# Kernel tuning notes

Measured on AMD Instinct MI355X. Metric: run time of the kernel, lower is better.

Reference implementation:

```python
import jax, jax.numpy as jnp
import numpy as np

B, S, D, H = 4, 2048, 1024, 16
DK = D // H
NEG = -1000000000.0


def setup_inputs() -> dict:
    key = jax.random.key(0)
    ks = jax.random.split(key, 12)
    scale = 1.0 / np.sqrt(D)
    inp = {
        "query": jax.random.normal(ks[0], (B, S, D), jnp.float32),
        "key": jax.random.normal(ks[1], (B, S, D), jnp.float32),
        "value": jax.random.normal(ks[2], (B, S, D), jnp.float32),
        "mask": jax.random.randint(ks[3], (B, S, S), 0, 2, jnp.int32),
        "Wq": jax.random.normal(ks[4], (D, D), jnp.float32) * scale,
        "bq": jnp.zeros((D,), jnp.float32),
        "Wk": jax.random.normal(ks[5], (D, D), jnp.float32) * scale,
        "bk": jnp.zeros((D,), jnp.float32),
        "Wv": jax.random.normal(ks[6], (D, D), jnp.float32) * scale,
        "bv": jnp.zeros((D,), jnp.float32),
        "Wo": jax.random.normal(ks[7], (D, D), jnp.float32) * scale,
        "bo": jnp.zeros((D,), jnp.float32),
    }
    return inp


def _split_heads(x):
    # (B, S, D) -> (B, H, S, DK)
    return x.reshape(B, -1, H, DK).transpose(0, 2, 1, 3)


def reference(query, key, value, mask, Wq, bq, Wk, bk, Wv, bv, Wo, bo):
    q = _split_heads(query @ Wq.T + bq)
    k = _split_heads(key @ Wk.T + bk)
    v = _split_heads(value @ Wv.T + bv)
    scores = jnp.einsum('bhqd,bhkd->bhqk', q, k) / jnp.sqrt(jnp.float32(DK))
    scores = jnp.where(mask[:, None, :, :] == 0, NEG, scores)
    p_attn = jax.nn.softmax(scores, axis=-1)
    x = jnp.einsum('bhqk,bhkd->bhqd', p_attn, v)
    x = x.transpose(0, 2, 1, 3).reshape(B, -1, D)
    return x @ Wo.T + bo
```

## Files before the change

### kernel.cpp

```cpp
#include <hip/hip_runtime.h>

#define BDIM 4
#define SDIM 2048
#define DDIM 1024
#define HDIM 16
#define DKDIM 64
#define MDIM (BDIM*SDIM)

typedef __attribute__((ext_vector_type(8))) short bf16x8_t;
typedef __attribute__((ext_vector_type(4))) float f32x4_t;
typedef __attribute__((ext_vector_type(16))) float f32x16_t;

__device__ __forceinline__ unsigned short f2bf(float f) {
    union { float f; unsigned u; } v; v.f = f;
    unsigned r = v.u + 0x7FFFu + ((v.u >> 16) & 1u);
    return (unsigned short)(r >> 16);
}

__device__ __forceinline__ unsigned pkbf(float a, float b) {
    unsigned r;
    asm("v_cvt_pk_bf16_f32 %0, %1, %2" : "=v"(r) : "v"(a), "v"(b));
    return r;
}

__device__ __forceinline__ void plswap(unsigned &a, unsigned &b) {
    asm("v_permlane32_swap_b32 %0, %1" : "+v"(a), "+v"(b));
}

#if defined(__has_builtin) && __has_builtin(__builtin_amdgcn_exp2f)
#define EXP2F(x) __builtin_amdgcn_exp2f(x)
#else
#define EXP2F(x) __expf((x) * 0.69314718f)
#endif

#if defined(__has_builtin) && __has_builtin(__builtin_amdgcn_sbfe)
#define SBFE1(x, p) __builtin_amdgcn_sbfe((int)(x), (p), 1)
#else
#define SBFE1(x, p) (((int)((x) << (31 - (p)))) >> 31)
#endif

#define QSCALE 0.18033688011112042f

__device__ __forceinline__ void gl_lds16(const void* g, void* l) {
    __builtin_amdgcn_global_load_lds(
        (const __attribute__((address_space(1))) unsigned int*)g,
        (__attribute__((address_space(3))) unsigned int*)l, 16, 0, 0);
}

__global__ void cvt3(const float* __restrict__ a, const float* __restrict__ b, const float* __restrict__ c,
                     unsigned short* __restrict__ oa, unsigned short* __restrict__ ob, unsigned short* __restrict__ oc,
                     int n4) {
    int i = blockIdx.x * blockDim.x + threadIdx.x;
    const float* s = blockIdx.y == 0 ? a : (blockIdx.y == 1 ? b : c);
    unsigned short* d = blockIdx.y == 0 ? oa : (blockIdx.y == 1 ? ob : oc);
    if (i < n4) {
        float4 v = ((const float4*)s)[i];
        uint2 o;
        o.x = pkbf(v.x, v.y);
        o.y = pkbf(v.z, v.w);
        ((uint2*)d)[i] = o;
    }
}

__global__ void cvt4(const float* __restrict__ a, const float* __restrict__ b,
                     const float* __restrict__ c, const float* __restrict__ e,
                     unsigned short* __restrict__ oa, unsigned short* __restrict__ ob,
                     unsigned short* __restrict__ oc, unsigned short* __restrict__ oe,
                     int n4) {
    int i = blockIdx.x * blockDim.x + threadIdx.x;
    const float* s = blockIdx.y == 0 ? a : (blockIdx.y == 1 ? b : (blockIdx.y == 2 ? c : e));
    unsigned short* d = blockIdx.y == 0 ? oa : (blockIdx.y == 1 ? ob : (blockIdx.y == 2 ? oc : oe));
    if (i < n4) {
        float4 v = ((const float4*)s)[i];
        uint2 o;
        o.x = pkbf(v.x, v.y);
        o.y = pkbf(v.z, v.w);
        ((uint2*)d)[i] = o;
    }
}

__global__ void pack_mask(const int* __restrict__ m, unsigned long long* __restrict__ bits) {
    int g = blockIdx.x * 256 + threadIdx.x;
    unsigned long long bal = __ballot(m[g] != 0);
    if ((threadIdx.x & 63) == 0) bits[g >> 6] = bal;
}

__global__ __launch_bounds__(256) void gemm_qkv(
    const unsigned short* __restrict__ A0, const unsigned short* __restrict__ A1,
    const unsigned short* __restrict__ A2,
    const unsigned short* __restrict__ B0, const unsigned short* __restrict__ B1,
    const unsigned short* __restrict__ B2,
    const float* __restrict__ bi0, const float* __restrict__ bi1, const float* __restrict__ bi2,
    unsigned short* __restrict__ C0, unsigned short* __restrict__ C1,
    unsigned short* __restrict__ C2)
{
    __shared__ unsigned short As[2][128 * 32];
    __shared__ unsigned short Bs[2][128 * 32];
    const int K = DDIM, M = MDIM, N = DDIM;
    const int bid = blockIdx.x;
    const int swz = (bid & 7) * 192 + (bid >> 3);
    const int z = swz >> 9;
    const int rem = swz & 511;
    const int bm = rem >> 3, bn = rem & 7;

    const unsigned short* A = z == 0 ? A0 : (z == 1 ? A1 : A2);
    const unsigned short* Bw = z == 0 ? B0 : (z == 1 ? B1 : B2);
    const float* bias = z == 0 ? bi0 : (z == 1 ? bi1 : bi2);
    unsigned short* Cb = z == 0 ? C0 : (z == 1 ? C1 : C2);
    const float scale = z == 0 ? QSCALE : 1.0f;

    const int tid = threadIdx.x;
    const int w = tid >> 6, lane = tid & 63;
    const int wr = w >> 1, wc = w & 1;
    const int quad = lane >> 4, l16 = lane & 15;

    const int rl = lane >> 2;
    const int cl = (((lane & 3) ^ ((rl >> 1) & 3)) * 8);
    const int sw = (l16 >> 1) & 3;
    const int c0 = w * 2;
    const unsigned short* gA = A + (size_t)(bm * 128 + c0 * 16 + rl) * K + cl;
    const unsigned short* gB = Bw + (size_t)(bn * 128 + c0 * 16 + rl) * K + cl;
    const int ldsoff = c0 * 512 + lane * 8;

    f32x4_t acc[4][4] = {};

    gl_lds16(gA, &As[0][ldsoff]);
    gl_lds16(gA + (size_t)16 * K, &As[0][ldsoff + 16 * 32]);
    gl_lds16(gB, &Bs[0][ldsoff]);
    gl_lds16(gB + (size_t)16 * K, &Bs[0][ldsoff + 16 * 32]);

    int cur = 0;
    for (int k0 = 0; k0 < K; k0 += 32) {
        __syncthreads();
        if (k0 + 32 < K) {
            const unsigned short* nA = gA + k0 + 32;
            const unsigned short* nB = gB + k0 + 32;
            gl_lds16(nA, &As[cur ^ 1][ldsoff]);
            gl_lds16(nA + (size_t)16 * K, &As[cur ^ 1][ldsoff + 16 * 32]);
            gl_lds16(nB, &Bs[cur ^ 1][ldsoff]);
            gl_lds16(nB + (size_t)16 * K, &Bs[cur ^ 1][ldsoff + 16 * 32]);
        }
        bf16x8_t af[4], bfr[4];
#pragma unroll
        for (int mi = 0; mi < 4; ++mi)
            af[mi] = *(const bf16x8_t*)(&As[cur][(wr * 64 + mi * 16 + l16) * 32 + (quad ^ sw) * 8]);
#pragma unroll
        for (int ni = 0; ni < 4; ++ni)
            bfr[ni] = *(const bf16x8_t*)(&Bs[cur][(wc * 64 + ni * 16 + l16) * 32 + (quad ^ sw) * 8]);
#pragma unroll
        for (int mi = 0; mi < 4; ++mi)
#pragma unroll
            for (int ni = 0; ni < 4; ++ni)
                acc[mi][ni] = __builtin_amdgcn_mfma_f32_16x16x32_bf16(bfr[ni], af[mi], acc[mi][ni], 0, 0, 0);
        cur ^= 1;
    }

    if (z == 2) {
#pragma unroll
        for (int mi = 0; mi < 4; ++mi) {
#pragma unroll
            for (int ni = 0; ni < 4; ++ni) {
                const int n0 = bn * 128 + wc * 64 + ni * 16 + quad * 4;
                const int m = bm * 128 + wr * 64 + mi * 16 + l16;
                const float4 bv4 = *(const float4*)&bias[n0];
                Cb[(size_t)(n0 + 0) * M + m] = f2bf(acc[mi][ni][0] + bv4.x);
                Cb[(size_t)(n0 + 1) * M + m] = f2bf(acc[mi][ni][1] + bv4.y);
                Cb[(size_t)(n0 + 2) * M + m] = f2bf(acc[mi][ni][2] + bv4.z);
                Cb[(size_t)(n0 + 3) * M + m] = f2bf(acc[mi][ni][3] + bv4.w);
            }
        }
    } else {
#pragma unroll
        for (int mi = 0; mi < 4; ++mi) {
#pragma unroll
            for (int ni = 0; ni < 4; ++ni) {
                const int n0 = bn * 128 + wc * 64 + ni * 16 + quad * 4;
                const int m = bm * 128 + wr * 64 + mi * 16 + l16;
                const float4 bv4 = *(const float4*)&bias[n0];
                uint2 pk2;
                pk2.x = pkbf((acc[mi][ni][0] + bv4.x) * scale, (acc[mi][ni][1] + bv4.y) * scale);
                pk2.y = pkbf((acc[mi][ni][2] + bv4.z) * scale, (acc[mi][ni][3] + bv4.w) * scale);
                *(uint2*)(Cb + (size_t)m * N + n0) = pk2;
            }
        }
    }
}

__global__ __launch_bounds__(256) void gemm_out(
    const unsigned short* __restrict__ A,
    const unsigned short* __restrict__ Bw,
    const float* __restrict__ bias,
    float* __restrict__ Cf)
{
    __shared__ unsigned short As[2][128 * 32];
    __shared__ unsigned short Bs[2][128 * 32];
    const int K = DDIM, N = DDIM;
    const int bid = blockIdx.x;
    const int swz = (bid & 7) * 64 + (bid >> 3);
    const int bm = swz >> 3, bn = swz & 7;
    const int tid = threadIdx.x;
    const int w = tid >> 6, lane = tid & 63;
    const int wr = w >> 1, wc = w & 1;
    const int quad = lane >> 4, l16 = lane & 15;

    const int rl = lane >> 2;
    const int cl = (((lane & 3) ^ ((rl >> 1) & 3)) * 8);
    const int sw = (l16 >> 1) & 3;
    const int c0 = w * 2;
    const unsigned short* gA = A + (size_t)(bm * 128 + c0 * 16 + rl) * K + cl;
    const unsigned short* gB = Bw + (size_t)(bn * 128 + c0 * 16 + rl) * K + cl;
    const int ldsoff = c0 * 512 + lane * 8;

    f32x4_t acc[4][4] = {};

    gl_lds16(gA, &As[0][ldsoff]);
    gl_lds16(gA + (size_t)16 * K, &As[0][ldsoff + 16 * 32]);
    gl_lds16(gB, &Bs[0][ldsoff]);
    gl_lds16(gB + (size_t)16 * K, &Bs[0][ldsoff + 16 * 32]);

    int cur = 0;
    for (int k0 = 0; k0 < K; k0 += 32) {
        __syncthreads();
        if (k0 + 32 < K) {
            const unsigned short* nA = gA + k0 + 32;
            const unsigned short* nB = gB + k0 + 32;
            gl_lds16(nA, &As[cur ^ 1][ldsoff]);
            gl_lds16(nA + (size_t)16 * K, &As[cur ^ 1][ldsoff + 16 * 32]);
            gl_lds16(nB, &Bs[cur ^ 1][ldsoff]);
            gl_lds16(nB + (size_t)16 * K, &Bs[cur ^ 1][ldsoff + 16 * 32]);
        }
        bf16x8_t af[4], bfr[4];
#pragma unroll
        for (int mi = 0; mi < 4; ++mi)
            af[mi] = *(const bf16x8_t*)(&As[cur][(wr * 64 + mi * 16 + l16) * 32 + (quad ^ sw) * 8]);
#pragma unroll
        for (int ni = 0; ni < 4; ++ni)
            bfr[ni] = *(const bf16x8_t*)(&Bs[cur][(wc * 64 + ni * 16 + l16) * 32 + (quad ^ sw) * 8]);
#pragma unroll
        for (int mi = 0; mi < 4; ++mi)
#pragma unroll
            for (int ni = 0; ni < 4; ++ni)
                acc[mi][ni] = __builtin_amdgcn_mfma_f32_16x16x32_bf16(bfr[ni], af[mi], acc[mi][ni], 0, 0, 0);
        cur ^= 1;
    }

#pragma unroll
    for (int mi = 0; mi < 4; ++mi) {
#pragma unroll
        for (int ni = 0; ni < 4; ++ni) {
            const int n0 = bn * 128 + wc * 64 + ni * 16 + quad * 4;
            const int m = bm * 128 + wr * 64 + mi * 16 + l16;
            const float4 bv4 = *(const float4*)&bias[n0];
            float4 o;
            o.x = acc[mi][ni][0] + bv4.x;
            o.y = acc[mi][ni][1] + bv4.y;
            o.z = acc[mi][ni][2] + bv4.z;
            o.w = acc[mi][ni][3] + bv4.w;
            *(float4*)(Cf + (size_t)m * N + n0) = o;
        }
    }
}

__global__ __launch_bounds__(256, 4) void attn_kernel(
    const unsigned short* __restrict__ Qp,
    const unsigned short* __restrict__ Kp,
    const unsigned short* __restrict__ Vt,
    const unsigned long long* __restrict__ mbits,
    unsigned short* __restrict__ Xa)
{
    __shared__ unsigned short SMEM[16384];
    const int tid = threadIdx.x, w = tid >> 6, lane = tid & 63;
    const int l32 = lane & 31, hi = lane >> 5;
    const int bid = blockIdx.x;
    const int swz = (bid & 7) * 128 + (bid >> 3);
    const int qt = swz & 15, h = (swz >> 4) & 15, b = swz >> 8;
    const int q0 = qt * 128;
    const int rl = lane >> 2;
    const int cl = (((lane & 3) ^ ((rl >> 1) & 3)) * 8);
    const int swl = (l32 >> 1) & 3;
    const int lbase = (l32 >> 4) * 512 + (l32 & 15) * 32 + ((hi ^ swl) * 8);
    const int myq = b * SDIM + q0 + w * 32 + l32;

    bf16x8_t qf[4];
    {
        const unsigned short* gq = Qp + (size_t)myq * DDIM + h * 64 + hi * 8;
#pragma unroll
        for (int c = 0; c < 4; ++c)
            qf[c] = *(const bf16x8_t*)(gq + c * 16);
    }

    const unsigned long long* mq = mbits + (size_t)myq * 32;

    const int cc0 = w * 2, cc1 = w * 2 + 1;
    const unsigned short* gK0 = Kp + (size_t)(b * SDIM + (cc0 & 3) * 16 + rl) * DDIM + h * 64 + (cc0 >> 2) * 32 + cl;
    const unsigned short* gK1 = Kp + (size_t)(b * SDIM + (cc1 & 3) * 16 + rl) * DDIM + h * 64 + (cc1 >> 2) * 32 + cl;
    const unsigned short* gV0 = Vt + (size_t)(h * 64 + (cc0 & 3) * 16 + rl) * MDIM + b * SDIM + (cc0 >> 2) * 32 + cl;
    const unsigned short* gV1 = Vt + (size_t)(h * 64 + (cc1 & 3) * 16 + rl) * MDIM + b * SDIM + (cc1 >> 2) * 32 + cl;
    unsigned short* dK0 = SMEM + cc0 * 512 + lane * 8;
    unsigned short* dK1 = SMEM + cc1 * 512 + lane * 8;
    unsigned short* dV0 = SMEM + 8192 + cc0 * 512 + lane * 8;
    unsigned short* dV1 = SMEM + 8192 + cc1 * 512 + lane * 8;

    gl_lds16(gK0, dK0);
    gl_lds16(gK1, dK1);
    gl_lds16(gV0, dV0);
    gl_lds16(gV1, dV1);
    unsigned long long nm = mq[0];

    f32x16_t o0 = {}, o1 = {}, o4 = {};
    union { unsigned u[4]; bf16x8_t v; } ones;
    ones.u[0] = ones.u[1] = ones.u[2] = ones.u[3] = 0x3F803F80u;

    int cur = 0;
    for (int kt = 0; kt < SDIM / 64; ++kt) {
        __syncthreads();
        const unsigned long long mysh = nm >> (4 * hi);
        const unsigned mw0 = (unsigned)mysh;
        const unsigned mw1 = (unsigned)(mysh >> 32);

        if (kt + 1 < SDIM / 64) {
            const int nb = (cur ^ 1) * 4096;
            const size_t ko = (size_t)(kt + 1) * 64 * DDIM;
            const size_t vo = (size_t)(kt + 1) * 64;
            gl_lds16(gK0 + ko, dK0 + nb);
            gl_lds16(gK1 + ko, dK1 + nb);
            gl_lds16(gV0 + vo, dV0 + nb);
            gl_lds16(gV1 + vo, dV1 + nb);
            nm = mq[kt + 1];
        }
        const unsigned short* Ksb = SMEM + cur * 4096;
        const unsigned short* Vsb = SMEM + 8192 + cur * 4096;

#pragma unroll
        for (int t = 0; t < 2; ++t) {
            f32x16_t s = {};
            __builtin_amdgcn_s_setprio(1);
#pragma unroll
            for (int c = 0; c < 4; ++c) {
                const bf16x8_t ak = *(const bf16x8_t*)(Ksb + (c >> 1) * 2048 + t * 1024 + (lbase ^ ((c & 1) * 16)));
                s = __builtin_amdgcn_mfma_f32_32x32x16_bf16(ak, qf[c], s, 0, 0, 0);
            }
            __builtin_amdgcn_s_setprio(0);
            const unsigned wm = t ? mw1 : mw0;
            float p[16];
#pragma unroll
            for (int r = 0; r < 16; ++r) {
                const int pos = (r & 3) + 8 * (r >> 2);
                const float pe = EXP2F(s[r]);
                const int mm = SBFE1(wm, pos);
                p[r] = __uint_as_float(__float_as_uint(pe) & (unsigned)mm);
            }
#pragma unroll
            for (int c2 = 0; c2 < 2; ++c2) {
                unsigned d0 = pkbf(p[c2 * 8 + 0], p[c2 * 8 + 1]);
                unsigned d1 = pkbf(p[c2 * 8 + 2], p[c2 * 8 + 3]);
                unsigned d2 = pkbf(p[c2 * 8 + 4], p[c2 * 8 + 5]);
                unsigned d3 = pkbf(p[c2 * 8 + 6], p[c2 * 8 + 7]);
                plswap(d0, d2);
                plswap(d1, d3);
                union { unsigned u[4]; bf16x8_t v; } pf;
                pf.u[0] = d0; pf.u[1] = d1; pf.u[2] = d2; pf.u[3] = d3;
                const bf16x8_t va0 = *(const bf16x8_t*)(Vsb + t * 2048 + (lbase ^ (c2 * 16)));
                const bf16x8_t va1 = *(const bf16x8_t*)(Vsb + t * 2048 + 1024 + (lbase ^ (c2 * 16)));
                __builtin_amdgcn_s_setprio(1);
                o0 = __builtin_amdgcn_mfma_f32_32x32x16_bf16(va0, pf.v, o0, 0, 0, 0);
                o1 = __builtin_amdgcn_mfma_f32_32x32x16_bf16(va1, pf.v, o1, 0, 0, 0);
                o4 = __builtin_amdgcn_mfma_f32_32x32x16_bf16(ones.v, pf.v, o4, 0, 0, 0);
                __builtin_amdgcn_s_setprio(0);
            }
        }
        cur ^= 1;
    }

    __syncthreads();
    unsigned short* T = SMEM + w * 2304;
    const float rcp = 1.0f / o4[0];
#pragma unroll
    for (int pi = 0; pi < 8; ++pi) {
        const int dk = (pi & 1) * 2 + 8 * (pi >> 1) + 4 * hi;
        *(unsigned*)&T[l32 * 72 + dk]      = pkbf(o0[2 * pi] * rcp, o0[2 * pi + 1] * rcp);
        *(unsigned*)&T[l32 * 72 + 32 + dk] = pkbf(o1[2 * pi] * rcp, o1[2 * pi + 1] * rcp);
    }
    const int rrow = lane >> 1;
    const unsigned short* Trow = SMEM + w * 2304 + rrow * 72 + (lane & 1) * 32;
    unsigned short* dst = Xa + (size_t)(b * SDIM + q0 + w * 32 + rrow) * DDIM + h * 64 + (lane & 1) * 32;
#pragma unroll
    for (int i = 0; i < 4; ++i)
        *(bf16x8_t*)(dst + i * 8) = *(const bf16x8_t*)(Trow + i * 8);
}

extern "C" void kernel_launch(void* const* d_in, const int* in_sizes, int n_in,
                              void* d_out, int out_size, void* d_ws, size_t ws_size,
                              hipStream_t stream)
{
    const float* query = (const float*)d_in[0];
    const float* key   = (const float*)d_in[1];
    const float* value = (const float*)d_in[2];
    const int*   mask  = (const int*)d_in[3];
    const float* Wq = (const float*)d_in[4];  const float* bq = (const float*)d_in[5];
    const float* Wk = (const float*)d_in[6];  const float* bk = (const float*)d_in[7];
    const float* Wv = (const float*)d_in[8];  const float* bv = (const float*)d_in[9];
    const float* Wo = (const float*)d_in[10]; const float* bo = (const float*)d_in[11];

    const size_t MD = (size_t)MDIM * DDIM;
    const size_t DD = (size_t)DDIM * DDIM;

    unsigned short* qb  = (unsigned short*)d_ws;
    unsigned short* kb  = qb + MD;
    unsigned short* vb  = kb + MD;
    unsigned short* wqb = vb + MD;
    unsigned short* wkb = wqb + DD;
    unsigned short* wvb = wkb + DD;
    unsigned short* wob = wvb + DD;
    unsigned short* Qp  = wob + DD;
    unsigned short* Kp  = Qp + MD;
    unsigned short* Vt  = Kp + MD;
    unsigned short* Xa  = Vt + MD;
    unsigned long long* mbits = (unsigned long long*)qb;

    {
        const int n4m = (int)(MD / 4), n4d = (int)(DD / 4);
        dim3 g3((n4m + 255) / 256, 3), g4((n4d + 255) / 256, 4);
        cvt3<<<g3, 256, 0, stream>>>(query, key, value, qb, kb, vb, n4m);
        cvt4<<<g4, 256, 0, stream>>>(Wq, Wk, Wv, Wo, wqb, wkb, wvb, wob, n4d);
    }

    gemm_qkv<<<1536, 256, 0, stream>>>(qb, kb, vb, wqb, wkb, wvb, bq, bk, bv, Qp, Kp, Vt);

    pack_mask<<<(BDIM * SDIM * SDIM) / 256, 256, 0, stream>>>(mask, mbits);

    attn_kernel<<<BDIM * HDIM * (SDIM / 128), 256, 0, stream>>>(Qp, Kp, Vt, mbits, Xa);

    gemm_out<<<512, 256, 0, stream>>>(Xa, wob, bo, (float*)d_out);
}
```

Measured before the change: 419.2 us.

## Load K and V fragments directly from global memory instead of staging through LDS

The attention kernel stops staging K and V tiles in shared memory with double-buffered async copies and barriers. Each wave now reads its MFMA operand fragments for K and transposed V straight from global memory into registers, and the mask word is loaded per iteration. This removes the per-tile __syncthreads and LDS traffic and shrinks shared memory to the epilogue transpose buffer, which may raise occupancy. In exchange, every wave re-reads the same K/V data from global memory and cache (four times per block), with no explicit prefetch to hide load latency.

After: 600.0 us. 43.1% more time.

```diff
diff --git a/kernel.cpp b/kernel.cpp
--- a/kernel.cpp
+++ b/kernel.cpp
@@ -268,17 +268,13 @@
     const unsigned long long* __restrict__ mbits,
     unsigned short* __restrict__ Xa)
 {
-    __shared__ unsigned short SMEM[16384];
+    __shared__ unsigned short SMEM[4 * 2304];
     const int tid = threadIdx.x, w = tid >> 6, lane = tid & 63;
     const int l32 = lane & 31, hi = lane >> 5;
     const int bid = blockIdx.x;
     const int swz = (bid & 7) * 128 + (bid >> 3);
     const int qt = swz & 15, h = (swz >> 4) & 15, b = swz >> 8;
     const int q0 = qt * 128;
-    const int rl = lane >> 2;
-    const int cl = (((lane & 3) ^ ((rl >> 1) & 3)) * 8);
-    const int swl = (l32 >> 1) & 3;
-    const int lbase = (l32 >> 4) * 512 + (l32 & 15) * 32 + ((hi ^ swl) * 8);
     const int myq = b * SDIM + q0 + w * 32 + l32;
 
     bf16x8_t qf[4];
@@ -291,56 +287,42 @@
 
     const unsigned long long* mq = mbits + (size_t)myq * 32;
 
-    const int cc0 = w * 2, cc1 = w * 2 + 1;
-    const unsigned short* gK0 = Kp + (size_t)(b * SDIM + (cc0 & 3) * 16 + rl) * DDIM + h * 64 + (cc0 >> 2) * 32 + cl;
-    const unsigned short* gK1 = Kp + (size_t)(b * SDIM + (cc1 & 3) * 16 + rl) * DDIM + h * 64 + (cc1 >> 2) * 32 + cl;
-    const unsigned short* gV0 = Vt + (size_t)(h * 64 + (cc0 & 3) * 16 + rl) * MDIM + b * SDIM + (cc0 >> 2) * 32 + cl;
-    const unsigned short* gV1 = Vt + (size_t)(h * 64 + (cc1 & 3) * 16 + rl) * MDIM + b * SDIM + (cc1 >> 2) * 32 + cl;
-    unsigned short* dK0 = SMEM + cc0 * 512 + lane * 8;
-    unsigned short* dK1 = SMEM + cc1 * 512 + lane * 8;
-    unsigned short* dV0 = SMEM + 8192 + cc0 * 512 + lane * 8;
-    unsigned short* dV1 = SMEM + 8192 + cc1 * 512 + lane * 8;
-
-    gl_lds16(gK0, dK0);
-    gl_lds16(gK1, dK1);
-    gl_lds16(gV0, dV0);
-    gl_lds16(gV1, dV1);
-    unsigned long long nm = mq[0];
+    const unsigned short* Kb = Kp + (size_t)(b * SDIM + l32) * DDIM + h * 64 + hi * 8;
+    const unsigned short* Vb0 = Vt + (size_t)(h * 64 + l32) * MDIM + b * SDIM + hi * 8;
+    const unsigned short* Vb1 = Vb0 + (size_t)32 * MDIM;
 
     f32x16_t o0 = {}, o1 = {}, o4 = {};
     union { unsigned u[4]; bf16x8_t v; } ones;
     ones.u[0] = ones.u[1] = ones.u[2] = ones.u[3] = 0x3F803F80u;
 
-    int cur = 0;
     for (int kt = 0; kt < SDIM / 64; ++kt) {
-        __syncthreads();
+        const unsigned long long nm = mq[kt];
         const unsigned long long mysh = nm >> (4 * hi);
         const unsigned mw0 = (unsigned)mysh;
         const unsigned mw1 = (unsigned)(mysh >> 32);
 
-        if (kt + 1 < SDIM / 64) {
-            const int nb = (cur ^ 1) * 4096;
-            const size_t ko = (size_t)(kt + 1) * 64 * DDIM;
-            const size_t vo = (size_t)(kt + 1) * 64;
-            gl_lds16(gK0 + ko, dK0 + nb);
-            gl_lds16(gK1 + ko, dK1 + nb);
-            gl_lds16(gV0 + vo, dV0 + nb);
-            gl_lds16(gV1 + vo, dV1 + nb);
-            nm = mq[kt + 1];
-        }
-        const unsigned short* Ksb = SMEM + cur * 4096;
-        const unsigned short* Vsb = SMEM + 8192 + cur * 4096;
-
 #pragma unroll
         for (int t = 0; t < 2; ++t) {
+            const int key0 = kt * 64 + t * 32;
+            const unsigned short* Kr = Kb + (size_t)key0 * DDIM;
+            const unsigned short* Vr0 = Vb0 + key0;
+            const unsigned short* Vr1 = Vb1 + key0;
+            bf16x8_t ak[4];
+#pragma unroll
+            for (int c = 0; c < 4; ++c)
+                ak[c] = *(const bf16x8_t*)(Kr + c * 16);
+            bf16x8_t va00 = *(const bf16x8_t*)(Vr0);
+            bf16x8_t va01 = *(const bf16x8_t*)(Vr0 + 16);
+            bf16x8_t va10 = *(const bf16x8_t*)(Vr1);
+            bf16x8_t va11 = *(const bf16x8_t*)(Vr1 + 16);
+
             f32x16_t s = {};
             __builtin_amdgcn_s_setprio(1);
 #pragma unroll
-            for (int c = 0; c < 4; ++c) {
-                const bf16x8_t ak = *(const bf16x8_t*)(Ksb + (c >> 1) * 2048 + t * 1024 + (lbase ^ ((c & 1) * 16)));
-                s = __builtin_amdgcn_mfma_f32_32x32x16_bf16(ak, qf[c], s, 0, 0, 0);
-            }
+            for (int c = 0; c < 4; ++c)
+                s = __builtin_amdgcn_mfma_f32_32x32x16_bf16(ak[c], qf[c], s, 0, 0, 0);
             __builtin_amdgcn_s_setprio(0);
+
             const unsigned wm = t ? mw1 : mw0;
             float p[16];
 #pragma unroll
@@ -360,8 +342,8 @@
                 plswap(d1, d3);
                 union { unsigned u[4]; bf16x8_t v; } pf;
                 pf.u[0] = d0; pf.u[1] = d1; pf.u[2] = d2; pf.u[3] = d3;
-                const bf16x8_t va0 = *(const bf16x8_t*)(Vsb + t * 2048 + (lbase ^ (c2 * 16)));
-                const bf16x8_t va1 = *(const bf16x8_t*)(Vsb + t * 2048 + 1024 + (lbase ^ (c2 * 16)));
+                const bf16x8_t va0 = c2 ? va01 : va00;
+                const bf16x8_t va1 = c2 ? va11 : va10;
                 __builtin_amdgcn_s_setprio(1);
                 o0 = __builtin_amdgcn_mfma_f32_32x32x16_bf16(va0, pf.v, o0, 0, 0, 0);
                 o1 = __builtin_amdgcn_mfma_f32_32x32x16_bf16(va1, pf.v, o1, 0, 0, 0);
@@ -369,10 +351,8 @@
                 __builtin_amdgcn_s_setprio(0);
             }
         }
-        cur ^= 1;
-    }
-
-    __syncthreads();
+    }
+
     unsigned short* T = SMEM + w * 2304;
     const float rcp = 1.0f / o4[0];
 #pragma unroll
```
